# Kernel tuning notes

Measured on AMD Instinct MI355X. Metric: run time of the kernel, lower is better.

The kernel has to match this reference:

```python
import jax, jax.numpy as jnp
import numpy as np

N_TOKENS = 8192
IN_FEATURES = 4096
OUT_FEATURES = 4096


def setup_inputs() -> dict:
    key = jax.random.key(0)
    kx, kw, ks = jax.random.split(key, 3)
    x = jax.random.normal(kx, (N_TOKENS, IN_FEATURES), dtype=jnp.float32)
    # int8 weight in [-127, 126], per torch.randint(-127, 127, ...)
    weight = jax.random.randint(kw, (OUT_FEATURES, IN_FEATURES), -127, 127, dtype=jnp.int32).astype(jnp.int8)
    weight_scales = jax.random.uniform(ks, (OUT_FEATURES,), dtype=jnp.float32, minval=0.001, maxval=0.01)
    bias = jnp.zeros((1, OUT_FEATURES), dtype=jnp.float32)
    return {"x": x, "weight": weight, "weight_scales": weight_scales, "bias": bias}


def reference(x, weight, weight_scales, bias):
    # --- dynamic per-token activation quantization (min-max / abs-max) ---
    # scale per token so that max |x| maps to 127
    x_absmax = jnp.max(jnp.abs(x), axis=-1, keepdims=True)          # [T, 1]
    x_scale = x_absmax / 127.0                                       # [T, 1]
    q_x = jnp.clip(jnp.round(x / x_scale), -127, 127).astype(jnp.int8)  # [T, K]

    # --- int8 GEMM with int32 accumulation: q_y = q_x @ weight.T ---
    q_y = jax.lax.dot_general(
        q_x, weight,
        dimension_numbers=(((1,), (1,)), ((), ())),
        preferred_element_type=jnp.int32,
    )                                                                # [T, N] int32

    # --- dequantize: per-channel weight scale x per-token activation scale ---
    y = q_y.astype(jnp.float32) * weight_scales[None, :] * x_scale   # [T, N]
    y = y + bias
    return y
```

## Files before the change

kernel.cpp:

```cpp
#include <hip/hip_runtime.h>
#include <cstdint>
#include <cstddef>

#define T_TOKENS 8192
#define K_DIM 4096
#define N_DIM 4096
#define K_TILES 32

#define PACK_BLOCKS (N_DIM * K_DIM / 4 / 256)
#define QUANT_BLOCKS T_TOKENS

using i32x4 = __attribute__((ext_vector_type(4))) int;

__global__ __launch_bounds__(256) void prep(const int* __restrict__ win,
                                            int8_t* __restrict__ wout,
                                            const float* __restrict__ x,
                                            int8_t* __restrict__ qx,
                                            float* __restrict__ xscale) {
    const int bid = blockIdx.x;
    const int tid = threadIdx.x;

    if (bid < PACK_BLOCKS) {
        const int idx = bid * 256 + tid;
        const i32x4 v = reinterpret_cast<const i32x4*>(win)[idx];
        uint32_t pk = (uint32_t)(v.x & 255) | ((uint32_t)(v.y & 255) << 8) |
                      ((uint32_t)(v.z & 255) << 16) | ((uint32_t)(v.w & 255) << 24);
        reinterpret_cast<int*>(wout)[idx] = (int)pk;
        return;
    }

    const int t = bid - PACK_BLOCKS;
    const float4* row = reinterpret_cast<const float4*>(x + (size_t)t * K_DIM);

    float4 v[4];
    float amax = 0.0f;
#pragma unroll
    for (int i = 0; i < 4; ++i) {
        v[i] = row[i * 256 + tid];
        amax = fmaxf(amax, fabsf(v[i].x));
        amax = fmaxf(amax, fabsf(v[i].y));
        amax = fmaxf(amax, fabsf(v[i].z));
        amax = fmaxf(amax, fabsf(v[i].w));
    }
#pragma unroll
    for (int off = 32; off > 0; off >>= 1)
        amax = fmaxf(amax, __shfl_xor(amax, off));

    __shared__ float red[4];
    if ((tid & 63) == 0) red[tid >> 6] = amax;
    __syncthreads();
    amax = fmaxf(fmaxf(red[0], red[1]), fmaxf(red[2], red[3]));

    const float scale = fmaxf(amax, 1e-30f) * (1.0f / 127.0f);
    if (tid == 0) xscale[t] = scale;

    const float inv = 1.0f / scale;
    int* qrow = reinterpret_cast<int*>(qx + (size_t)t * K_DIM);
#pragma unroll
    for (int i = 0; i < 4; ++i) {
        int q0 = (int)fminf(fmaxf(rintf(v[i].x * inv), -127.0f), 127.0f);
        int q1 = (int)fminf(fmaxf(rintf(v[i].y * inv), -127.0f), 127.0f);
        int q2 = (int)fminf(fmaxf(rintf(v[i].z * inv), -127.0f), 127.0f);
        int q3 = (int)fminf(fmaxf(rintf(v[i].w * inv), -127.0f), 127.0f);
        uint32_t pk = (uint32_t)(q0 & 255) | ((uint32_t)(q1 & 255) << 8) |
                      ((uint32_t)(q2 & 255) << 16) | ((uint32_t)(q3 & 255) << 24);
        qrow[i * 256 + tid] = (int)pk;
    }
}

__global__ __launch_bounds__(512, 2) void int8_gemm(const int8_t* __restrict__ qx,
                                                    const int8_t* __restrict__ w,
                                                    const float* __restrict__ xscale,
                                                    const float* __restrict__ wscale,
                                                    const float* __restrict__ bias,
                                                    float* __restrict__ out) {
    extern __shared__ int8_t lds[];

    const int tid = threadIdx.x;
    const int lane = tid & 63;
    const int wave = tid >> 6;
    const int wr = wave >> 2;
    const int wn = wave & 3;
    const int l16 = lane & 15;
    const int quad = lane >> 4;

    const int wg = ((blockIdx.x & 7) << 6) | ((int)blockIdx.x >> 3);
    const int tm = wg >> 4;
    const int tn = wg & 15;

    const int8_t* gA = qx + (size_t)tm * 256 * K_DIM;
    const int8_t* gB = w + (size_t)tn * 256 * K_DIM;

    const int s_row = tid >> 2;
    const int scol = (((tid & 3) ^ ((s_row >> 1) & 3)) << 4);
    const int fcol = ((quad ^ ((l16 >> 1) & 3)) << 4);

    const int ldsA_rd = (wr * 128 + l16) * 64 + fcol;
    const int ldsB_rd = 32768 + (wn * 64 + l16) * 64 + fcol;

#define STAGE2(buf, op, ksl, k0)                                                        \
    {                                                                                   \
        const int8_t* g_ = ((op) ? gB : gA) +                                           \
                           ((size_t)s_row * K_DIM + (size_t)((k0) + (ksl) * 64 + scol));\
        int8_t* l_ = lds + (buf) * 65536 + (op) * 32768 + (ksl) * 16384 + tid * 16;     \
        __builtin_amdgcn_global_load_lds(                                               \
            (const __attribute__((address_space(1))) void*)g_,                          \
            (__attribute__((address_space(3))) void*)l_, 16, 0, 0);                     \
        __builtin_amdgcn_global_load_lds(                                               \
            (const __attribute__((address_space(1))) void*)(g_ + (size_t)128 * K_DIM),  \
            (__attribute__((address_space(3))) void*)(l_ + 8192), 16, 0, 0);            \
    }

    i32x4 acc[8][4] = {};
    i32x4 af[4], bf[4];

#define READ_B(buf, ksl)                                                     \
    {                                                                        \
        const int8_t* sB_ = lds + (buf) * 65536 + (ksl) * 16384 + ldsB_rd;   \
        _Pragma("unroll") for (int nj = 0; nj < 4; ++nj)                     \
            bf[nj] = *(const i32x4*)(sB_ + nj * 1024);                       \
    }
#define READ_A(buf, ksl, mh)                                                 \
    {                                                                        \
        const int8_t* sA_ =                                                  \
            lds + (buf) * 65536 + (ksl) * 16384 + (mh) * 4096 + ldsA_rd;     \
        _Pragma("unroll") for (int q = 0; q < 4; ++q)                        \
            af[q] = *(const i32x4*)(sA_ + q * 1024);                         \
    }
#define MFMA16(mh)                                                           \
    __builtin_amdgcn_s_setprio(1);                                           \
    _Pragma("unroll") for (int q = 0; q < 4; ++q) {                          \
        _Pragma("unroll") for (int nj = 0; nj < 4; ++nj)                     \
            acc[(mh) * 4 + q][nj] = __builtin_amdgcn_mfma_i32_16x16x64_i8(   \
                af[q], bf[nj], acc[(mh) * 4 + q][nj], 0, 0, 0);              \
    }                                                                        \
    __builtin_amdgcn_s_setprio(0);

    STAGE2(0, 0, 0, 0)
    STAGE2(0, 1, 0, 0)
    STAGE2(0, 0, 1, 0)
    STAGE2(0, 1, 1, 0)

    for (int t = 0; t < K_TILES - 1; ++t) {
        const int cur = t & 1;
        const int nxt = cur ^ 1;
        const int k1 = (t + 1) << 7;

        STAGE2(nxt, 0, 0, k1)
        STAGE2(nxt, 1, 0, k1)
        STAGE2(nxt, 0, 1, k1)
        STAGE2(nxt, 1, 1, k1)
        asm volatile("s_waitcnt vmcnt(8)" ::: "memory");
        __builtin_amdgcn_s_barrier();

        READ_B(cur, 0)
        READ_A(cur, 0, 0)
        MFMA16(0)
        READ_A(cur, 0, 1)
        __builtin_amdgcn_s_barrier();

        MFMA16(1)
        READ_B(cur, 1)
        READ_A(cur, 1, 0)
        __builtin_amdgcn_s_barrier();

        MFMA16(0)
        READ_A(cur, 1, 1)
        __builtin_amdgcn_s_barrier();

        MFMA16(1)
        __builtin_amdgcn_s_barrier();
    }

    {
        asm volatile("s_waitcnt vmcnt(0)" ::: "memory");
        __builtin_amdgcn_s_barrier();
        READ_B(1, 0)
        READ_A(1, 0, 0)
        MFMA16(0)
        READ_A(1, 0, 1)
        __builtin_amdgcn_s_barrier();
        MFMA16(1)
        READ_B(1, 1)
        READ_A(1, 1, 0)
        __builtin_amdgcn_s_barrier();
        MFMA16(0)
        READ_A(1, 1, 1)
        __builtin_amdgcn_s_barrier();
        MFMA16(1)
    }

    const int row_base = tm * 256 + wr * 128 + quad * 4;
    const int col_base = tn * 256 + wn * 64 + l16;
    float wsv[4], bsv[4];
#pragma unroll
    for (int nj = 0; nj < 4; ++nj) {
        wsv[nj] = wscale[col_base + nj * 16];
        bsv[nj] = bias[col_base + nj * 16];
    }
#pragma unroll
    for (int mi = 0; mi < 8; ++mi) {
#pragma unroll
        for (int r = 0; r < 4; ++r) {
            const int trow = row_base + mi * 16 + r;
            const float xs = xscale[trow];
            float* orow = out + (size_t)trow * N_DIM + col_base;
#pragma unroll
            for (int nj = 0; nj < 4; ++nj)
                orow[nj * 16] = (float)acc[mi][nj][r] * (wsv[nj] * xs) + bsv[nj];
        }
    }
#undef STAGE2
#undef READ_B
#undef READ_A
#undef MFMA16
}

extern "C" void kernel_launch(void* const* d_in, const int* in_sizes, int n_in,
                              void* d_out, int out_size, void* d_ws, size_t ws_size,
                              hipStream_t stream) {
    const float* x = (const float*)d_in[0];
    const int* w_i32 = (const int*)d_in[1];
    const float* wscale = (const float*)d_in[2];
    const float* bias = (const float*)d_in[3];
    float* out = (float*)d_out;

    int8_t* qx = (int8_t*)d_ws;
    float* xscale = (float*)((char*)d_ws + (size_t)T_TOKENS * K_DIM);
    int8_t* wpk = (int8_t*)((char*)d_ws + (size_t)T_TOKENS * K_DIM + 65536);

    static bool attr_set = false;
    if (!attr_set) {
        (void)hipFuncSetAttribute(reinterpret_cast<const void*>(&int8_gemm),
                                  hipFuncAttributeMaxDynamicSharedMemorySize, 131072);
        attr_set = true;
    }

    prep<<<PACK_BLOCKS + QUANT_BLOCKS, 256, 0, stream>>>(w_i32, wpk, x, qx, xscale);

    int8_gemm<<<dim3(512), dim3(512), 131072, stream>>>(qx, wpk, xscale, wscale, bias, out);
}
```

Before: 403.9 us.

## Double workgroup to 16 waves with 64x64 per-wave tiles and split staging

Raises the GEMM workgroup to 1024 threads so each of 16 waves computes a 64x64 output tile instead of 128x64, halving per-wave accumulators. Each thread now issues a single async global-to-LDS load per stage, and the K-loop interleaves staging of each half of the next tile with compute on the current half. This aims to improve latency hiding and reduce register pressure. In exchange, each wave issues fewer MFMAs per LDS fragment load and the loop synchronises with more barriers.

```diff
diff --git a/kernel.cpp b/kernel.cpp
--- a/kernel.cpp
+++ b/kernel.cpp
@@ -68,12 +68,12 @@
     }
 }
 
-__global__ __launch_bounds__(512, 2) void int8_gemm(const int8_t* __restrict__ qx,
-                                                    const int8_t* __restrict__ w,
-                                                    const float* __restrict__ xscale,
-                                                    const float* __restrict__ wscale,
-                                                    const float* __restrict__ bias,
-                                                    float* __restrict__ out) {
+__global__ __launch_bounds__(1024, 4) void int8_gemm(const int8_t* __restrict__ qx,
+                                                     const int8_t* __restrict__ w,
+                                                     const float* __restrict__ xscale,
+                                                     const float* __restrict__ wscale,
+                                                     const float* __restrict__ bias,
+                                                     float* __restrict__ out) {
     extern __shared__ int8_t lds[];
 
     const int tid = threadIdx.x;
@@ -95,10 +95,10 @@
     const int scol = (((tid & 3) ^ ((s_row >> 1) & 3)) << 4);
     const int fcol = ((quad ^ ((l16 >> 1) & 3)) << 4);
 
-    const int ldsA_rd = (wr * 128 + l16) * 64 + fcol;
+    const int ldsA_rd = (wr * 64 + l16) * 64 + fcol;
     const int ldsB_rd = 32768 + (wn * 64 + l16) * 64 + fcol;
 
-#define STAGE2(buf, op, ksl, k0)                                                        \
+#define STAGE1(buf, op, ksl, k0)                                                        \
     {                                                                                   \
         const int8_t* g_ = ((op) ? gB : gA) +                                           \
                            ((size_t)s_row * K_DIM + (size_t)((k0) + (ksl) * 64 + scol));\
@@ -106,91 +106,69 @@
         __builtin_amdgcn_global_load_lds(                                               \
             (const __attribute__((address_space(1))) void*)g_,                          \
             (__attribute__((address_space(3))) void*)l_, 16, 0, 0);                     \
-        __builtin_amdgcn_global_load_lds(                                               \
-            (const __attribute__((address_space(1))) void*)(g_ + (size_t)128 * K_DIM),  \
-            (__attribute__((address_space(3))) void*)(l_ + 8192), 16, 0, 0);            \
-    }
-
-    i32x4 acc[8][4] = {};
+    }
+
+    i32x4 acc[4][4] = {};
     i32x4 af[4], bf[4];
 
-#define READ_B(buf, ksl)                                                     \
+#define READ_AB(buf, ksl)                                                    \
     {                                                                        \
+        const int8_t* sA_ = lds + (buf) * 65536 + (ksl) * 16384 + ldsA_rd;   \
         const int8_t* sB_ = lds + (buf) * 65536 + (ksl) * 16384 + ldsB_rd;   \
+        _Pragma("unroll") for (int mi = 0; mi < 4; ++mi)                     \
+            af[mi] = *(const i32x4*)(sA_ + mi * 1024);                       \
         _Pragma("unroll") for (int nj = 0; nj < 4; ++nj)                     \
             bf[nj] = *(const i32x4*)(sB_ + nj * 1024);                       \
     }
-#define READ_A(buf, ksl, mh)                                                 \
-    {                                                                        \
-        const int8_t* sA_ =                                                  \
-            lds + (buf) * 65536 + (ksl) * 16384 + (mh) * 4096 + ldsA_rd;     \
-        _Pragma("unroll") for (int q = 0; q < 4; ++q)                        \
-            af[q] = *(const i32x4*)(sA_ + q * 1024);                         \
-    }
-#define MFMA16(mh)                                                           \
+#define MFMA16()                                                             \
     __builtin_amdgcn_s_setprio(1);                                           \
-    _Pragma("unroll") for (int q = 0; q < 4; ++q) {                          \
+    _Pragma("unroll") for (int mi = 0; mi < 4; ++mi) {                       \
         _Pragma("unroll") for (int nj = 0; nj < 4; ++nj)                     \
-            acc[(mh) * 4 + q][nj] = __builtin_amdgcn_mfma_i32_16x16x64_i8(   \
-                af[q], bf[nj], acc[(mh) * 4 + q][nj], 0, 0, 0);              \
+            acc[mi][nj] = __builtin_amdgcn_mfma_i32_16x16x64_i8(             \
+                af[mi], bf[nj], acc[mi][nj], 0, 0, 0);                       \
     }                                                                        \
     __builtin_amdgcn_s_setprio(0);
 
-    STAGE2(0, 0, 0, 0)
-    STAGE2(0, 1, 0, 0)
-    STAGE2(0, 0, 1, 0)
-    STAGE2(0, 1, 1, 0)
+    STAGE1(0, 0, 0, 0)
+    STAGE1(0, 1, 0, 0)
+    STAGE1(0, 0, 1, 0)
+    STAGE1(0, 1, 1, 0)
 
     for (int t = 0; t < K_TILES - 1; ++t) {
         const int cur = t & 1;
         const int nxt = cur ^ 1;
         const int k1 = (t + 1) << 7;
 
-        STAGE2(nxt, 0, 0, k1)
-        STAGE2(nxt, 1, 0, k1)
-        STAGE2(nxt, 0, 1, k1)
-        STAGE2(nxt, 1, 1, k1)
-        asm volatile("s_waitcnt vmcnt(8)" ::: "memory");
-        __builtin_amdgcn_s_barrier();
-
-        READ_B(cur, 0)
-        READ_A(cur, 0, 0)
-        MFMA16(0)
-        READ_A(cur, 0, 1)
-        __builtin_amdgcn_s_barrier();
-
-        MFMA16(1)
-        READ_B(cur, 1)
-        READ_A(cur, 1, 0)
-        __builtin_amdgcn_s_barrier();
-
-        MFMA16(0)
-        READ_A(cur, 1, 1)
-        __builtin_amdgcn_s_barrier();
-
-        MFMA16(1)
+        STAGE1(nxt, 0, 0, k1)
+        STAGE1(nxt, 1, 0, k1)
+        asm volatile("s_waitcnt vmcnt(4)" ::: "memory");
+        __builtin_amdgcn_s_barrier();
+        READ_AB(cur, 0)
+        MFMA16()
+        __builtin_amdgcn_s_barrier();
+
+        STAGE1(nxt, 0, 1, k1)
+        STAGE1(nxt, 1, 1, k1)
+        asm volatile("s_waitcnt vmcnt(4)" ::: "memory");
+        __builtin_amdgcn_s_barrier();
+        READ_AB(cur, 1)
+        MFMA16()
         __builtin_amdgcn_s_barrier();
     }
 
     {
+        asm volatile("s_waitcnt vmcnt(2)" ::: "memory");
+        __builtin_amdgcn_s_barrier();
+        READ_AB(1, 0)
+        MFMA16()
+        __builtin_amdgcn_s_barrier();
         asm volatile("s_waitcnt vmcnt(0)" ::: "memory");
         __builtin_amdgcn_s_barrier();
-        READ_B(1, 0)
-        READ_A(1, 0, 0)
-        MFMA16(0)
-        READ_A(1, 0, 1)
-        __builtin_amdgcn_s_barrier();
-        MFMA16(1)
-        READ_B(1, 1)
-        READ_A(1, 1, 0)
-        __builtin_amdgcn_s_barrier();
-        MFMA16(0)
-        READ_A(1, 1, 1)
-        __builtin_amdgcn_s_barrier();
-        MFMA16(1)
-    }
-
-    const int row_base = tm * 256 + wr * 128 + quad * 4;
+        READ_AB(1, 1)
+        MFMA16()
+    }
+
+    const int row_base = tm * 256 + wr * 64 + quad * 4;
     const int col_base = tn * 256 + wn * 64 + l16;
     float wsv[4], bsv[4];
 #pragma unroll
@@ -199,7 +177,7 @@
         bsv[nj] = bias[col_base + nj * 16];
     }
 #pragma unroll
-    for (int mi = 0; mi < 8; ++mi) {
+    for (int mi = 0; mi < 4; ++mi) {
 #pragma unroll
         for (int r = 0; r < 4; ++r) {
             const int trow = row_base + mi * 16 + r;
@@ -210,9 +188,8 @@
                 orow[nj * 16] = (float)acc[mi][nj][r] * (wsv[nj] * xs) + bsv[nj];
         }
     }
-#undef STAGE2
-#undef READ_B
-#undef READ_A
+#undef STAGE1
+#undef READ_AB
 #undef MFMA16
 }
 
@@ -238,5 +215,5 @@
 
     prep<<<PACK_BLOCKS + QUANT_BLOCKS, 256, 0, stream>>>(w_i32, wpk, x, qx, xscale);
 
-    int8_gemm<<<dim3(512), dim3(512), 131072, stream>>>(qx, wpk, xscale, wscale, bias, out);
+    int8_gemm<<<dim3(512), dim3(1024), 131072, stream>>>(qx, wpk, xscale, wscale, bias, out);
 }
```

After: 394.4 us. 2.3% less time.
